# Optimization experiments

Hardware: AMD Instinct MI355X
Metric: run time of the kernel (lower is better)

The kernel has to match this reference:

```python
import jax, jax.numpy as jnp
import numpy as np

N = 100000
E = 1600000
D_IN = 128
H1 = 128
H2 = 128
C = 64


def setup_inputs() -> dict:
    key = jax.random.key(0)
    ks = jax.random.split(key, 10)
    x_content = jax.random.normal(ks[0], (N, D_IN), dtype=jnp.float32)
    edge_index = jax.random.randint(ks[1], (2, E), 0, N, dtype=jnp.int64)
    # SAGEConv params: lin_l (applied to aggregated neighbors, has bias),
    # lin_r (applied to root node, no bias). Kaiming-ish scaling.
    def lin(k, fan_in, fan_out):
        return jax.random.normal(k, (fan_in, fan_out), dtype=jnp.float32) / np.sqrt(fan_in)
    return {
        "x_content": x_content,
        "edge_index": edge_index,
        "W1l": lin(ks[2], D_IN, H1),
        "b1": jnp.zeros((H1,), jnp.float32),
        "W1r": lin(ks[3], D_IN, H1),
        "W2l": lin(ks[4], H1, H2),
        "b2": jnp.zeros((H2,), jnp.float32),
        "W2r": lin(ks[5], H1, H2),
        "Wout": lin(ks[6], H2, C),
        "bout": jnp.zeros((C,), jnp.float32),
    }


def _sage_conv(x, src, dst, Wl, b, Wr):
    # mean-aggregate neighbor features (messages flow src -> dst), then
    # out = mean_agg @ Wl + b + x @ Wr  (PyG SAGEConv, aggr='mean')
    msgs = x[src]                                            # [E, d]
    agg = jax.ops.segment_sum(msgs, dst, num_segments=N)     # [N, d]
    deg = jax.ops.segment_sum(jnp.ones((src.shape[0],), x.dtype), dst, num_segments=N)
    mean = agg / jnp.clip(deg, 1.0)[:, None]
    return mean @ Wl + b + x @ Wr


def reference(x_content, edge_index, W1l, b1, W1r, W2l, b2, W2r, Wout, bout):
    src, dst = edge_index[0], edge_index[1]
    # dropout is identity in eval mode (training=False)
    x = jax.nn.relu(_sage_conv(x_content, src, dst, W1l, b1, W1r))
    x = jax.nn.relu(_sage_conv(x, src, dst, W2l, b2, W2r))
    return x @ Wout + bout
```

## Files before the change

kernel.cpp:

```cpp
#include <hip/hip_runtime.h>
#include <hip/hip_fp8.h>

#define DD 128
#define CC 64
#define BKW 512
#define NPB 4096

typedef __attribute__((ext_vector_type(8))) short short8v;
typedef __attribute__((ext_vector_type(4))) float f32x4;
typedef __attribute__((ext_vector_type(2))) float f32x2;

static __device__ inline ushort f2bf_rne(float f) {
    unsigned u = __float_as_uint(f);
    unsigned r = (u + 0x7FFFu + ((u >> 16) & 1u)) >> 16;
    return (ushort)r;
}
static __device__ inline float bf2f(ushort h) {
    return __uint_as_float(((unsigned)h) << 16);
}

__global__ __launch_bounds__(256) void bucket_cnt_kernel(const int* __restrict__ ei,
                                                         int* __restrict__ bcnt, int E) {
    __shared__ int h[256];
    const int t = threadIdx.x;
    h[t] = 0;
    __syncthreads();
    const int base = blockIdx.x * 8192;
    const int end = min(E, base + 8192);
    for (int j = base + t; j < end; j += 256) {
        atomicAdd(&h[ei[E + j] >> 9], 1);
    }
    __syncthreads();
    if (h[t]) atomicAdd(&bcnt[t], h[t]);
}

__global__ __launch_bounds__(256) void bucket_scan_kernel(const int* __restrict__ bcnt,
                                                          int* __restrict__ boffs,
                                                          int* __restrict__ bcur) {
    __shared__ int s[256];
    const int t = threadIdx.x;
    int v = bcnt[t];
    s[t] = v;
    __syncthreads();
    for (int off = 1; off < 256; off <<= 1) {
        int xv = 0;
        if (t >= off) xv = s[t - off];
        __syncthreads();
        if (t >= off) s[t] += xv;
        __syncthreads();
    }
    int excl = s[t] - v;
    boffs[t] = excl;
    bcur[t] = excl;
    if (t == 255) boffs[256] = s[255];
}

__global__ __launch_bounds__(256) void binA_kernel(const int* __restrict__ ei,
                                                   int* __restrict__ bcur,
                                                   uint* __restrict__ ebuf, int E) {
    __shared__ int sRun[256];
    __shared__ int sRel[256];
    __shared__ int sBase[256];
    __shared__ uint sPair[NPB];
    __shared__ unsigned char sBkt[NPB];
    __shared__ int sHist[256];
    const int t = threadIdx.x;
    const int e0 = blockIdx.x * NPB;
    const int cntE = min(NPB, E - e0);

    sHist[t] = 0;
    __syncthreads();
    for (int j = t; j < cntE; j += 256) {
        int dst = ei[E + e0 + j];
        atomicAdd(&sHist[dst >> 9], 1);
    }
    __syncthreads();
    int h = sHist[t];
    sRun[t] = h;
    __syncthreads();
    for (int off = 1; off < 256; off <<= 1) {
        int v = 0;
        if (t >= off) v = sRun[t - off];
        __syncthreads();
        if (t >= off) sRun[t] += v;
        __syncthreads();
    }
    int runstart = sRun[t] - h;
    int base = 0;
    if (h > 0) base = atomicAdd(&bcur[t], h);
    sRun[t] = runstart;
    sRel[t] = runstart;
    sBase[t] = base;
    __syncthreads();
    for (int j = t; j < cntE; j += 256) {
        int src = ei[e0 + j];
        int dst = ei[E + e0 + j];
        int b = dst >> 9;
        int slot = atomicAdd(&sRel[b], 1);
        sPair[slot] = (uint)src | ((uint)(dst & 511) << 17);
        sBkt[slot] = (unsigned char)b;
    }
    __syncthreads();
    for (int s = t; s < cntE; s += 256) {
        uint p = sPair[s];
        int b = (int)sBkt[s];
        int gpos = sBase[b] + (s - sRun[b]);
        ebuf[gpos] = p;
    }
}

__global__ __launch_bounds__(256) void binB2_kernel(const uint* __restrict__ ebuf,
                                                    const int* __restrict__ boffs,
                                                    int* __restrict__ offs,
                                                    int* __restrict__ csr, int n) {
    __shared__ int sCnt[BKW];
    __shared__ int sOffs[BKW];
    __shared__ int sScan[256];
    const int t = threadIdx.x;
    const int node0 = blockIdx.x * BKW;
    const int node1 = min(n, node0 + BKW);
    const int start = boffs[blockIdx.x];
    const int end = boffs[blockIdx.x + 1];

    sCnt[t] = 0; sCnt[t + 256] = 0;
    __syncthreads();
    for (int j = start + t; j < end; j += 256) {
        int d = (int)(ebuf[j] >> 17);
        atomicAdd(&sCnt[d], 1);
    }
    __syncthreads();
    int v0 = sCnt[2 * t], v1 = sCnt[2 * t + 1];
    int sum = v0 + v1;
    sScan[t] = sum;
    __syncthreads();
    for (int off = 1; off < 256; off <<= 1) {
        int xv = 0;
        if (t >= off) xv = sScan[t - off];
        __syncthreads();
        if (t >= off) sScan[t] += xv;
        __syncthreads();
    }
    int excl = sScan[t] - sum;
    sOffs[2 * t] = start + excl;
    sOffs[2 * t + 1] = start + excl + v0;
    __syncthreads();
    for (int i = t; i < BKW; i += 256) {
        int node = node0 + i;
        if (node < n) offs[node] = sOffs[i];
    }
    if (node1 == n && t == 0) offs[n] = end;
    __syncthreads();
    sCnt[t] = 0; sCnt[t + 256] = 0;
    __syncthreads();
    for (int j = start + t; j < end; j += 256) {
        uint p = ebuf[j];
        int d = (int)(p >> 17);
        int r = atomicAdd(&sCnt[d], 1);
        csr[sOffs[d] + r] = (int)(p & 0x1FFFFu);
    }
}

__global__ __launch_bounds__(256) void prep_kernel(
    const float* __restrict__ x, ushort* __restrict__ xh, uint* __restrict__ xq,
    const float* __restrict__ Wl1, const float* __restrict__ Wr1,
    const float* __restrict__ Wl2, const float* __restrict__ Wr2,
    const float* __restrict__ Wout,
    ushort* __restrict__ WTfrag1, ushort* __restrict__ WTfrag2,
    ushort* __restrict__ WoFrag, int nxblk) {
    const int t = threadIdx.x;
    const int bx = blockIdx.x;
    if (bx < nxblk) {
        int i = bx * 256 + t;
        float4 a = ((const float4*)x)[2 * i];
        float4 b = ((const float4*)x)[2 * i + 1];
        float vv[8] = {a.x, a.y, a.z, a.w, b.x, b.y, b.z, b.w};
        ushort r[8];
        uint q[8];
        #pragma unroll
        for (int j = 0; j < 8; ++j) {
            r[j] = f2bf_rne(vv[j]);
            q[j] = (uint)__hip_fp8_e4m3(vv[j]).__x;
        }
        uint4 o;
        o.x = (uint)r[0] | ((uint)r[1] << 16);
        o.y = (uint)r[2] | ((uint)r[3] << 16);
        o.z = (uint)r[4] | ((uint)r[5] << 16);
        o.w = (uint)r[6] | ((uint)r[7] << 16);
        ((uint4*)xh)[i] = o;
        uint2 oq;
        oq.x = q[0] | (q[1] << 8) | (q[2] << 16) | (q[3] << 24);
        oq.y = q[4] | (q[5] << 8) | (q[6] << 16) | (q[7] << 24);
        ((uint2*)xq)[i] = oq;
    } else if (bx < nxblk + 32) {
        int li = bx - nxblk;
        int layer = li >> 4;
        int idx = (li & 15) * 256 + t;
        const float* Wl = layer ? Wl2 : Wl1;
        const float* Wr = layer ? Wr2 : Wr1;
        ushort* dst = (layer ? WTfrag2 : WTfrag1) + (size_t)idx * 8;
        int lane = idx & 63, tt = (idx >> 6) & 7, s = idx >> 9;
        int col = tt * 16 + (lane & 15);
        int k0 = s * 32 + (lane >> 4) * 8;
        #pragma unroll
        for (int j = 0; j < 8; ++j) {
            int k = k0 + j;
            float v = (k < DD) ? Wl[k * DD + col] : Wr[(k - DD) * DD + col];
            dst[j] = f2bf_rne(v);
        }
    } else {
        int idx = (bx - nxblk - 32) * 256 + t;
        ushort* dst = WoFrag + (size_t)idx * 8;
        int lane = idx & 63, tt = (idx >> 6) & 3, kc = idx >> 8;
        int col = tt * 16 + (lane & 15);
        int k0 = kc * 32 + (lane >> 4) * 8;
        #pragma unroll
        for (int j = 0; j < 8; ++j) {
            dst[j] = f2bf_rne(Wout[(k0 + j) * CC + col]);
        }
    }
}

__global__ __launch_bounds__(256) void csr_agg8_kernel(
    const uint* __restrict__ xq, const int* __restrict__ offs,
    const int* __restrict__ csr, ushort* __restrict__ meanH, int n) {
    int node = blockIdx.x * 4 + (threadIdx.x >> 6);
    if (node >= n) return;
    const int lane = threadIdx.x & 63;
    const int sub = lane >> 4;
    const int li = lane & 15;
    const int start = offs[node];
    const int c = offs[node + 1] - start;
    f32x2 a[4], aa[4];
    #pragma unroll
    for (int k = 0; k < 4; ++k) { a[k] = (f32x2){0.f, 0.f}; aa[k] = (f32x2){0.f, 0.f}; }
    #define ACC8(A, U) { \
        A[0] += __builtin_amdgcn_cvt_pk_f32_fp8(U.x, false); \
        A[1] += __builtin_amdgcn_cvt_pk_f32_fp8(U.x, true);  \
        A[2] += __builtin_amdgcn_cvt_pk_f32_fp8(U.y, false); \
        A[3] += __builtin_amdgcn_cvt_pk_f32_fp8(U.y, true);  }
    const int c16 = c & ~15;
    int j = 0;
    if (c16 > 0) {
        int s0 = csr[start + sub];
        int s1 = csr[start + 4 + sub];
        int s2 = csr[start + 8 + sub];
        int s3 = csr[start + 12 + sub];
        for (; j < c16; j += 16) {
            int t0 = 0, t1 = 0, t2 = 0, t3 = 0;
            if (j + 16 < c16) {
                t0 = csr[start + j + 16 + sub];
                t1 = csr[start + j + 20 + sub];
                t2 = csr[start + j + 24 + sub];
                t3 = csr[start + j + 28 + sub];
            }
            uint2 u0 = *(const uint2*)((const uchar*)xq + (size_t)s0 * DD + li * 8);
            uint2 u1 = *(const uint2*)((const uchar*)xq + (size_t)s1 * DD + li * 8);
            uint2 u2 = *(const uint2*)((const uchar*)xq + (size_t)s2 * DD + li * 8);
            uint2 u3 = *(const uint2*)((const uchar*)xq + (size_t)s3 * DD + li * 8);
            ACC8(a, u0); ACC8(a, u1); ACC8(aa, u2); ACC8(aa, u3);
            s0 = t0; s1 = t1; s2 = t2; s3 = t3;
        }
    }
    if (c - j >= 8) {
        int s0 = csr[start + j + sub];
        int s1 = csr[start + j + 4 + sub];
        uint2 u0 = *(const uint2*)((const uchar*)xq + (size_t)s0 * DD + li * 8);
        uint2 u1 = *(const uint2*)((const uchar*)xq + (size_t)s1 * DD + li * 8);
        ACC8(a, u0); ACC8(aa, u1);
        j += 8;
    }
    if (c - j >= 4) {
        int s = csr[start + j + sub];
        uint2 u = *(const uint2*)((const uchar*)xq + (size_t)s * DD + li * 8);
        ACC8(a, u);
        j += 4;
    }
    if (j + sub < c) {
        int s = csr[start + j + sub];
        uint2 u = *(const uint2*)((const uchar*)xq + (size_t)s * DD + li * 8);
        ACC8(aa, u);
    }
    #undef ACC8
    float res[8];
    #pragma unroll
    for (int k = 0; k < 4; ++k) {
        f32x2 v = a[k] + aa[k];
        float e0 = v.x; e0 += __shfl_xor(e0, 16); e0 += __shfl_xor(e0, 32);
        float e1 = v.y; e1 += __shfl_xor(e1, 16); e1 += __shfl_xor(e1, 32);
        res[2 * k] = e0; res[2 * k + 1] = e1;
    }
    if (sub == 0) {
        float inv = 1.0f / fmaxf((float)c, 1.0f);
        short8v o;
        #pragma unroll
        for (int k = 0; k < 8; ++k) o[k] = (short)f2bf_rne(res[k] * inv);
        *(short8v*)(meanH + (size_t)node * DD + li * 8) = o;
    }
}

template <bool PROJ>
__global__ __launch_bounds__(256) void layer_mfma_kernel(
    const ushort* __restrict__ meanH, const ushort* __restrict__ rootH,
    const ushort* __restrict__ WTfrag, const float* __restrict__ bias,
    ushort* __restrict__ outH, uchar* __restrict__ outQ,
    const ushort* __restrict__ WoFrag, const float* __restrict__ bout,
    float* __restrict__ outF, int n, int ntiles) {
    __shared__ ushort sH[32][136];
    __shared__ uchar sQ[PROJ ? 1 : 32][PROJ ? 16 : 144];
    const int tid = threadIdx.x;
    const int w = tid >> 6;
    const int l = tid & 63;
    const int rh = w >> 1;
    const int ch = w & 1;
    const int lrow = rh * 16 + (l & 15);
    const int kb = (l >> 4) * 8;
    const int lcol = l & 15;
    const int lrow0 = rh * 16 + (l >> 4) * 4;

    short8v breg[8][4];
    #pragma unroll
    for (int s = 0; s < 8; ++s) {
        #pragma unroll
        for (int t = 0; t < 4; ++t) {
            breg[s][t] = *(const short8v*)(WTfrag + (size_t)s * 4096 +
                                           (ch * 4 + t) * 512 + l * 8);
        }
    }
    float bias_r[4];
    #pragma unroll
    for (int t = 0; t < 4; ++t) bias_r[t] = bias[ch * 64 + t * 16 + lcol];

    for (int tile = blockIdx.x; tile < ntiles; tile += gridDim.x) {
        const int row0 = tile * 32;
        const int arowg = min(row0 + lrow, n - 1);
        const ushort* Am = meanH + (size_t)arowg * DD;
        const ushort* Ar = rootH + (size_t)arowg * DD;
        short8v ap[8];
        #pragma unroll
        for (int s = 0; s < 8; ++s) {
            ap[s] = (s < 4) ? *(const short8v*)(Am + s * 32 + kb)
                            : *(const short8v*)(Ar + (s - 4) * 32 + kb);
        }
        f32x4 acc[4];
        #pragma unroll
        for (int t = 0; t < 4; ++t) acc[t] = (f32x4){0.f, 0.f, 0.f, 0.f};
        #pragma unroll
        for (int s = 0; s < 8; ++s) {
            #pragma unroll
            for (int t = 0; t < 4; ++t) {
                acc[t] = __builtin_amdgcn_mfma_f32_16x16x32_bf16(ap[s], breg[s][t],
                                                                 acc[t], 0, 0, 0);
            }
        }

        if (!PROJ) {
            #pragma unroll
            for (int t = 0; t < 4; ++t) {
                const int col = ch * 64 + t * 16 + lcol;
                #pragma unroll
                for (int r = 0; r < 4; ++r) {
                    float o = fmaxf(acc[t][r] + bias_r[t], 0.f);
                    sH[lrow0 + r][col] = f2bf_rne(o);
                    sQ[lrow0 + r][col] = __hip_fp8_e4m3(o).__x;
                }
            }
            __syncthreads();
            for (int i = tid; i < 512; i += 256) {
                int row = i >> 4, seg = i & 15;
                int grow = row0 + row;
                if (grow < n)
                    *(uint4*)(outH + (size_t)grow * DD + seg * 8) =
                        *(const uint4*)&sH[row][seg * 8];
            }
            {
                int row = tid >> 3, seg = tid & 7;
                int grow = row0 + row;
                if (grow < n)
                    *(uint4*)(outQ + (size_t)grow * DD + seg * 16) =
                        *(const uint4*)&sQ[row][seg * 16];
            }
            __syncthreads();
        } else {
            #pragma unroll
            for (int t = 0; t < 4; ++t) {
                const int col = ch * 64 + t * 16 + lcol;
                #pragma unroll
                for (int r = 0; r < 4; ++r) {
                    sH[lrow0 + r][col] = f2bf_rne(fmaxf(acc[t][r] + bias_r[t], 0.f));
                }
            }
            __syncthreads();
            f32x4 po[2];
            po[0] = (f32x4){0.f, 0.f, 0.f, 0.f};
            po[1] = (f32x4){0.f, 0.f, 0.f, 0.f};
            #pragma unroll
            for (int kc = 0; kc < 4; ++kc) {
                short8v ah = *(const short8v*)&sH[lrow][kc * 32 + kb];
                #pragma unroll
                for (int t2 = 0; t2 < 2; ++t2) {
                    short8v bh = *(const short8v*)(WoFrag + (size_t)kc * 2048 +
                                                   (ch * 2 + t2) * 512 + l * 8);
                    po[t2] = __builtin_amdgcn_mfma_f32_16x16x32_bf16(ah, bh,
                                                                     po[t2], 0, 0, 0);
                }
            }
            #pragma unroll
            for (int t2 = 0; t2 < 2; ++t2) {
                const int col = ch * 32 + t2 * 16 + lcol;
                const float b = bout[col];
                #pragma unroll
                for (int r = 0; r < 4; ++r) {
                    int grow = row0 + lrow0 + r;
                    if (grow < n) outF[(size_t)grow * CC + col] = po[t2][r] + b;
                }
            }
            __syncthreads();
        }
    }
}

extern "C" void kernel_launch(void* const* d_in, const int* in_sizes, int n_in,
                              void* d_out, int out_size, void* d_ws, size_t ws_size,
                              hipStream_t stream) {
    const float* x    = (const float*)d_in[0];
    const int*   ei   = (const int*)d_in[1];
    const float* W1l  = (const float*)d_in[2];
    const float* b1   = (const float*)d_in[3];
    const float* W1r  = (const float*)d_in[4];
    const float* W2l  = (const float*)d_in[5];
    const float* b2   = (const float*)d_in[6];
    const float* W2r  = (const float*)d_in[7];
    const float* Wout = (const float*)d_in[8];
    const float* bout = (const float*)d_in[9];
    float* out = (float*)d_out;
    const int n = in_sizes[0] / DD;
    const int E = in_sizes[1] / 2;
    const size_t NP = (size_t)n * DD;

    const int NBUCK = (n + BKW - 1) / BKW;

    int* offs  = (int*)d_ws;
    int* bcnt  = offs + 100352;
    int* boffs = bcnt + 256;
    int* bcur  = boffs + 512;
    int* csr   = bcur + 256;
    uint* ebuf = (uint*)(csr + 1600256);
    uint* xq   = ebuf;
    ushort* xh = (ushort*)((uchar*)xq + NP);
    ushort* meanH = xh + NP;
    ushort* h1h = meanH + NP;
    ushort* WTfrag1 = h1h + NP;
    ushort* WTfrag2 = WTfrag1 + 32768;
    ushort* WoFrag  = WTfrag2 + 32768;
    uchar* h1q = (uchar*)(WoFrag + 8192);

    hipMemsetAsync(bcnt, 0, sizeof(int) * 256, stream);
    bucket_cnt_kernel<<<(E + 8191) / 8192, 256, 0, stream>>>(ei, bcnt, E);
    bucket_scan_kernel<<<1, 256, 0, stream>>>(bcnt, boffs, bcur);
    binA_kernel<<<(E + NPB - 1) / NPB, 256, 0, stream>>>(ei, bcur, ebuf, E);
    binB2_kernel<<<NBUCK, 256, 0, stream>>>(ebuf, boffs, offs, csr, n);

    const int nxblk = (int)(NP / 8 / 256);
    prep_kernel<<<nxblk + 36, 256, 0, stream>>>(x, xh, xq, W1l, W1r, W2l, W2r,
                                                Wout, WTfrag1, WTfrag2, WoFrag, nxblk);

    const int ntiles = (n + 31) / 32;
    const int lgrid = 625;
    const int ablk = (n + 3) / 4;

    csr_agg8_kernel<<<ablk, 256, 0, stream>>>(xq, offs, csr, meanH, n);
    layer_mfma_kernel<false><<<lgrid, 256, 0, stream>>>(
        meanH, xh, WTfrag1, b1, h1h, h1q,
        (const ushort*)nullptr, (const float*)nullptr, (float*)nullptr, n, ntiles);

    csr_agg8_kernel<<<ablk, 256, 0, stream>>>((const uint*)h1q, offs, csr, meanH, n);
    layer_mfma_kernel<true><<<lgrid, 256, 0, stream>>>(
        meanH, h1h, WTfrag2, b2, (ushort*)nullptr, (uchar*)nullptr,
        WoFrag, bout, out, n, ntiles);
}
```

Baseline: 227.1 us.

## Use 16-row tiles with per-wave column slices to drop block barriers

Measured after the change: 220.0 us. -3.1%, faster.

```diff
diff --git a/kernel.cpp b/kernel.cpp
--- a/kernel.cpp
+++ b/kernel.cpp
@@ -305,34 +305,34 @@
     ushort* __restrict__ outH, uchar* __restrict__ outQ,
     const ushort* __restrict__ WoFrag, const float* __restrict__ bout,
     float* __restrict__ outF, int n, int ntiles) {
-    __shared__ ushort sH[32][136];
-    __shared__ uchar sQ[PROJ ? 1 : 32][PROJ ? 16 : 144];
+    __shared__ ushort sW[PROJ ? 1 : 4][16][40];
+    __shared__ __align__(16) uchar sQ[PROJ ? 1 : 4][16][48];
+    __shared__ ushort sH[PROJ ? 2 : 1][16][136];
     const int tid = threadIdx.x;
     const int w = tid >> 6;
     const int l = tid & 63;
-    const int rh = w >> 1;
-    const int ch = w & 1;
-    const int lrow = rh * 16 + (l & 15);
+    const int lrow16 = l & 15;
     const int kb = (l >> 4) * 8;
     const int lcol = l & 15;
-    const int lrow0 = rh * 16 + (l >> 4) * 4;
-
-    short8v breg[8][4];
+    const int lrow0 = (l >> 4) * 4;
+
+    short8v breg[8][2];
     #pragma unroll
     for (int s = 0; s < 8; ++s) {
         #pragma unroll
-        for (int t = 0; t < 4; ++t) {
+        for (int t = 0; t < 2; ++t) {
             breg[s][t] = *(const short8v*)(WTfrag + (size_t)s * 4096 +
-                                           (ch * 4 + t) * 512 + l * 8);
-        }
-    }
-    float bias_r[4];
+                                           (w * 2 + t) * 512 + l * 8);
+        }
+    }
+    float bias_r[2];
     #pragma unroll
-    for (int t = 0; t < 4; ++t) bias_r[t] = bias[ch * 64 + t * 16 + lcol];
-
-    for (int tile = blockIdx.x; tile < ntiles; tile += gridDim.x) {
-        const int row0 = tile * 32;
-        const int arowg = min(row0 + lrow, n - 1);
+    for (int t = 0; t < 2; ++t) bias_r[t] = bias[w * 32 + t * 16 + lcol];
+
+    int pp = 0;
+    for (int tile = blockIdx.x; tile < ntiles; tile += gridDim.x, pp ^= 1) {
+        const int row0 = tile * 16;
+        const int arowg = min(row0 + lrow16, n - 1);
         const ushort* Am = meanH + (size_t)arowg * DD;
         const ushort* Ar = rootH + (size_t)arowg * DD;
         short8v ap[8];
@@ -341,80 +341,66 @@
             ap[s] = (s < 4) ? *(const short8v*)(Am + s * 32 + kb)
                             : *(const short8v*)(Ar + (s - 4) * 32 + kb);
         }
-        f32x4 acc[4];
-        #pragma unroll
-        for (int t = 0; t < 4; ++t) acc[t] = (f32x4){0.f, 0.f, 0.f, 0.f};
+        f32x4 acc[2];
+        acc[0] = (f32x4){0.f, 0.f, 0.f, 0.f};
+        acc[1] = (f32x4){0.f, 0.f, 0.f, 0.f};
         #pragma unroll
         for (int s = 0; s < 8; ++s) {
-            #pragma unroll
-            for (int t = 0; t < 4; ++t) {
-                acc[t] = __builtin_amdgcn_mfma_f32_16x16x32_bf16(ap[s], breg[s][t],
-                                                                 acc[t], 0, 0, 0);
-            }
+            acc[0] = __builtin_amdgcn_mfma_f32_16x16x32_bf16(ap[s], breg[s][0],
+                                                             acc[0], 0, 0, 0);
+            acc[1] = __builtin_amdgcn_mfma_f32_16x16x32_bf16(ap[s], breg[s][1],
+                                                             acc[1], 0, 0, 0);
         }
 
         if (!PROJ) {
             #pragma unroll
-            for (int t = 0; t < 4; ++t) {
-                const int col = ch * 64 + t * 16 + lcol;
+            for (int t = 0; t < 2; ++t) {
                 #pragma unroll
                 for (int r = 0; r < 4; ++r) {
                     float o = fmaxf(acc[t][r] + bias_r[t], 0.f);
-                    sH[lrow0 + r][col] = f2bf_rne(o);
-                    sQ[lrow0 + r][col] = __hip_fp8_e4m3(o).__x;
+                    sW[w][lrow0 + r][t * 16 + lcol] = f2bf_rne(o);
+                    sQ[w][lrow0 + r][t * 16 + lcol] = __hip_fp8_e4m3(o).__x;
                 }
             }
-            __syncthreads();
-            for (int i = tid; i < 512; i += 256) {
-                int row = i >> 4, seg = i & 15;
+            {
+                int row = l >> 2, seg = l & 3;
                 int grow = row0 + row;
                 if (grow < n)
-                    *(uint4*)(outH + (size_t)grow * DD + seg * 8) =
-                        *(const uint4*)&sH[row][seg * 8];
-            }
-            {
-                int row = tid >> 3, seg = tid & 7;
+                    *(uint4*)(outH + (size_t)grow * DD + w * 32 + seg * 8) =
+                        *(const uint4*)&sW[w][row][seg * 8];
+            }
+            if (l < 32) {
+                int row = l >> 1, seg = l & 1;
                 int grow = row0 + row;
                 if (grow < n)
-                    *(uint4*)(outQ + (size_t)grow * DD + seg * 16) =
-                        *(const uint4*)&sQ[row][seg * 16];
-            }
-            __syncthreads();
+                    *(uint4*)(outQ + (size_t)grow * DD + w * 32 + seg * 16) =
+                        *(const uint4*)&sQ[w][row][seg * 16];
+            }
         } else {
             #pragma unroll
-            for (int t = 0; t < 4; ++t) {
-                const int col = ch * 64 + t * 16 + lcol;
+            for (int t = 0; t < 2; ++t) {
                 #pragma unroll
                 for (int r = 0; r < 4; ++r) {
-                    sH[lrow0 + r][col] = f2bf_rne(fmaxf(acc[t][r] + bias_r[t], 0.f));
+                    sH[pp][lrow0 + r][w * 32 + t * 16 + lcol] =
+                        f2bf_rne(fmaxf(acc[t][r] + bias_r[t], 0.f));
                 }
             }
             __syncthreads();
-            f32x4 po[2];
-            po[0] = (f32x4){0.f, 0.f, 0.f, 0.f};
-            po[1] = (f32x4){0.f, 0.f, 0.f, 0.f};
+            f32x4 po = (f32x4){0.f, 0.f, 0.f, 0.f};
             #pragma unroll
             for (int kc = 0; kc < 4; ++kc) {
-                short8v ah = *(const short8v*)&sH[lrow][kc * 32 + kb];
-                #pragma unroll
-                for (int t2 = 0; t2 < 2; ++t2) {
-                    short8v bh = *(const short8v*)(WoFrag + (size_t)kc * 2048 +
-                                                   (ch * 2 + t2) * 512 + l * 8);
-                    po[t2] = __builtin_amdgcn_mfma_f32_16x16x32_bf16(ah, bh,
-                                                                     po[t2], 0, 0, 0);
-                }
-            }
+                short8v ah = *(const short8v*)&sH[pp][lrow16][kc * 32 + kb];
+                short8v bh = *(const short8v*)(WoFrag + (size_t)kc * 2048 +
+                                               w * 512 + l * 8);
+                po = __builtin_amdgcn_mfma_f32_16x16x32_bf16(ah, bh, po, 0, 0, 0);
+            }
+            const int col = w * 16 + lcol;
+            const float b = bout[col];
             #pragma unroll
-            for (int t2 = 0; t2 < 2; ++t2) {
-                const int col = ch * 32 + t2 * 16 + lcol;
-                const float b = bout[col];
-                #pragma unroll
-                for (int r = 0; r < 4; ++r) {
-                    int grow = row0 + lrow0 + r;
-                    if (grow < n) outF[(size_t)grow * CC + col] = po[t2][r] + b;
-                }
-            }
-            __syncthreads();
+            for (int r = 0; r < 4; ++r) {
+                int grow = row0 + lrow0 + r;
+                if (grow < n) outF[(size_t)grow * CC + col] = po[r] + b;
+            }
         }
     }
 }
@@ -464,8 +450,8 @@
     prep_kernel<<<nxblk + 36, 256, 0, stream>>>(x, xh, xq, W1l, W1r, W2l, W2r,
                                                 Wout, WTfrag1, WTfrag2, WoFrag, nxblk);
 
-    const int ntiles = (n + 31) / 32;
-    const int lgrid = 625;
+    const int ntiles = (n + 15) / 16;
+    const int lgrid = 1024;
     const int ablk = (n + 3) / 4;
 
     csr_agg8_kernel<<<ablk, 256, 0, stream>>>(xq, offs, csr, meanH, n);
```
